# Optimization experiments

Hardware: AMD Instinct MI355X
Metric: run time of the kernel (lower is better)

The kernel has to match this reference:

```python
import jax, jax.numpy as jnp
import numpy as np

N = 50000
E = 800000
IN_C = 256
HID = 256
OUT_C = 128


def _glorot(key, fan_in, fan_out):
    lim = float(np.sqrt(6.0 / (fan_in + fan_out)))
    return jax.random.uniform(key, (fan_in, fan_out), jnp.float32, -lim, lim)


def setup_inputs() -> dict:
    key = jax.random.key(0)
    ks = jax.random.split(key, 10)
    x = jax.random.normal(ks[0], (N, IN_C), dtype=jnp.float32)
    edge_index = jax.random.randint(ks[1], (2, E), 0, N, dtype=jnp.int64)
    return {
        "x": x,
        "edge_index": edge_index,
        # layer 0 MLP: Linear(IN_C,HID)+ReLU+Linear(HID,HID)+ReLU
        "eps0": jnp.zeros((), jnp.float32),
        "W1_0": _glorot(ks[2], IN_C, HID),
        "b1_0": jnp.zeros((HID,), jnp.float32),
        "W2_0": _glorot(ks[3], HID, HID),
        "b2_0": jnp.zeros((HID,), jnp.float32),
        # layer 1 MLP: Linear(HID,HID)+ReLU+Linear(HID,OUT_C)
        "eps1": jnp.zeros((), jnp.float32),
        "W1_1": _glorot(ks[4], HID, HID),
        "b1_1": jnp.zeros((HID,), jnp.float32),
        "W2_1": _glorot(ks[5], HID, OUT_C),
        "b2_1": jnp.zeros((OUT_C,), jnp.float32),
    }


def _gin_layer(x, src, dst, eps, W1, b1, W2, b2, final_relu):
    # sum-aggregate messages x[src] into dst nodes
    agg = jax.ops.segment_sum(x[src], dst, num_segments=N)  # [N, d]
    h = (1.0 + eps) * x + agg
    h = jax.nn.relu(h @ W1 + b1)
    h = h @ W2 + b2
    return jax.nn.relu(h) if final_relu else h


def reference(x, edge_index, eps0, W1_0, b1_0, W2_0, b2_0, eps1, W1_1, b1_1, W2_1, b2_1):
    src, dst = edge_index[0], edge_index[1]
    h = _gin_layer(x, src, dst, eps0, W1_0, b1_0, W2_0, b2_0, final_relu=True)
    h = jax.nn.relu(h)  # model-level ReLU between layers
    h = _gin_layer(h, src, dst, eps1, W1_1, b1_1, W2_1, b2_1, final_relu=False)
    return jax.nn.log_softmax(h, axis=1)
```

## Files before the change

kernel.cpp:

```cpp
#include <hip/hip_runtime.h>

#define FDIM 256
#define OUTC 128
#define CAP  96
#define CURS 16
#define LDA 264
#define MROWS 128

typedef float floatx4 __attribute__((ext_vector_type(4)));
typedef __bf16 bf16x8 __attribute__((ext_vector_type(8)));

__device__ __forceinline__ unsigned short f2bf(float f) {
    union { float f; unsigned u; } v; v.f = f;
    unsigned r = v.u + 0x7FFF + ((v.u >> 16) & 1);
    return (unsigned short)(r >> 16);
}
__device__ __forceinline__ unsigned pack2(float a, float b) {
    return ((unsigned)f2bf(a)) | (((unsigned)f2bf(b)) << 16);
}
__device__ __forceinline__ unsigned q8b(float v, float rs) {
    int q = __float2int_rn(v * rs);
    q = (q < -127 ? -127 : (q > 127 ? 127 : q)) + 128;
    return (unsigned)q;
}
__device__ __forceinline__ float ub0(unsigned v) { float f; asm("v_cvt_f32_ubyte0 %0, %1" : "=v"(f) : "v"(v)); return f; }
__device__ __forceinline__ float ub1(unsigned v) { float f; asm("v_cvt_f32_ubyte1 %0, %1" : "=v"(f) : "v"(v)); return f; }
__device__ __forceinline__ float ub2(unsigned v) { float f; asm("v_cvt_f32_ubyte2 %0, %1" : "=v"(f) : "v"(v)); return f; }
__device__ __forceinline__ float ub3(unsigned v) { float f; asm("v_cvt_f32_ubyte3 %0, %1" : "=v"(f) : "v"(v)); return f; }

__global__ __launch_bounds__(256)
void prep_kernel(const int* __restrict__ src, const int* __restrict__ dst,
                 int* __restrict__ cursor, unsigned short* __restrict__ esrc2, int E,
                 const float* __restrict__ x, unsigned char* __restrict__ xq,
                 float* __restrict__ xs0, int total8,
                 const float* __restrict__ W1_0, const float* __restrict__ W2_0,
                 const float* __restrict__ W1_1, const float* __restrict__ W2_1,
                 unsigned short* __restrict__ w1f_0, unsigned short* __restrict__ w2f_0,
                 unsigned short* __restrict__ w1f_1, unsigned short* __restrict__ w2f_1) {
    int gid = blockIdx.x * 256 + threadIdx.x;
    if (gid < E) {
        int d = dst[gid];
        int pos = atomicAdd(&cursor[d * CURS], 1);
        if (pos < CAP) esrc2[d * CAP + pos] = (unsigned short)src[gid];
        return;
    }
    gid -= E;
    if (gid < total8) {
        const float4* p = (const float4*)(x + (size_t)gid * 8);
        float4 a = p[0], b = p[1];
        float m = fmaxf(fmaxf(fmaxf(fabsf(a.x), fabsf(a.y)), fmaxf(fabsf(a.z), fabsf(a.w))),
                        fmaxf(fmaxf(fabsf(b.x), fabsf(b.y)), fmaxf(fabsf(b.z), fabsf(b.w))));
        #pragma unroll
        for (int off = 1; off < 32; off <<= 1) m = fmaxf(m, __shfl_xor(m, off));
        float rs = (m > 0.f) ? 127.0f / m : 0.f;
        unsigned lo = q8b(a.x, rs) | (q8b(a.y, rs) << 8) |
                      (q8b(a.z, rs) << 16) | (q8b(a.w, rs) << 24);
        unsigned hi = q8b(b.x, rs) | (q8b(b.y, rs) << 8) |
                      (q8b(b.z, rs) << 16) | (q8b(b.w, rs) << 24);
        *(uint2*)(xq + (size_t)gid * 8) = make_uint2(lo, hi);
        if ((threadIdx.x & 31) == 0) xs0[gid >> 5] = m * (1.0f / 127.0f);
        return;
    }
    gid -= total8;
    const int S = FDIM * FDIM;
    const float* W; unsigned short* WF; int local, J, Ncols;
    if (gid < S)          { W = W1_0; WF = w1f_0; local = gid;         J = 4; Ncols = FDIM; }
    else if (gid < 2 * S) { W = W2_0; WF = w2f_0; local = gid - S;     J = 4; Ncols = FDIM; }
    else if (gid < 3 * S) { W = W1_1; WF = w1f_1; local = gid - 2 * S; J = 4; Ncols = FDIM; }
    else if (gid < 3 * S + FDIM * OUTC)
                          { W = W2_1; WF = w2f_1; local = gid - 3 * S; J = 2; Ncols = OUTC; }
    else return;
    int e    = local & 7;
    int lane = (local >> 3) & 63;
    int l15  = lane & 15;
    int quad = lane >> 4;
    int rest = local >> 9;
    int j  = rest % J;  rest /= J;
    int kc = rest & 7;
    int g  = rest >> 3;
    int n = g * (16 * J) + j * 16 + l15;
    int k = kc * 32 + quad * 8 + e;
    WF[local] = f2bf(W[(size_t)k * Ncols + n]);
}

__global__ __launch_bounds__(256)
void gather_q8_kernel(const unsigned char* __restrict__ q,
                      const float* __restrict__ qs,
                      const unsigned short* __restrict__ esrc2,
                      const int* __restrict__ cursor,
                      const float* __restrict__ epsp,
                      unsigned short* __restrict__ out, int N, float bias) {
    int node = __builtin_amdgcn_readfirstlane(
        (int)((blockIdx.x * blockDim.x + threadIdx.x) >> 6));
    int lane = threadIdx.x & 63;
    if (node >= N) return;
    int col = lane * 4;
    int beg = node * CAP;
    int cnt = cursor[node * CURS];
    if (cnt > CAP) cnt = CAP;

    float a4[4] = {0.f, 0.f, 0.f, 0.f};
    float scl_sum = 0.f;

    int e = 0;
    for (; e + 16 <= cnt; e += 16) {
        const uint4* ip = (const uint4*)(esrc2 + beg + e);
        uint4 i0 = ip[0], i1 = ip[1];
        unsigned iw[8] = {i0.x, i0.y, i0.z, i0.w, i1.x, i1.y, i1.z, i1.w};
        int s[16]; float sc[16];
        #pragma unroll
        for (int m = 0; m < 8; ++m) {
            s[2*m]   = __builtin_amdgcn_readfirstlane((int)(iw[m] & 0xffffu));
            s[2*m+1] = __builtin_amdgcn_readfirstlane((int)(iw[m] >> 16));
        }
        #pragma unroll
        for (int k = 0; k < 16; ++k) { sc[k] = qs[s[k]]; scl_sum += sc[k]; }
        unsigned v[16];
        #pragma unroll
        for (int k = 0; k < 16; ++k)
            v[k] = *(const unsigned*)(q + (size_t)s[k] * FDIM + col);
        #pragma unroll
        for (int k = 0; k < 16; ++k) {
            a4[0] = fmaf(sc[k], ub0(v[k]), a4[0]);
            a4[1] = fmaf(sc[k], ub1(v[k]), a4[1]);
            a4[2] = fmaf(sc[k], ub2(v[k]), a4[2]);
            a4[3] = fmaf(sc[k], ub3(v[k]), a4[3]);
        }
    }
    int rem = cnt - e;
    if (rem > 0) {
        const uint4* ip = (const uint4*)(esrc2 + beg + e);
        uint4 i0 = ip[0], i1 = ip[1];
        unsigned iw[8] = {i0.x, i0.y, i0.z, i0.w, i1.x, i1.y, i1.z, i1.w};
        int s[16]; float sc[16];
        #pragma unroll
        for (int m = 0; m < 8; ++m) {
            s[2*m]   = __builtin_amdgcn_readfirstlane((int)(iw[m] & 0xffffu));
            s[2*m+1] = __builtin_amdgcn_readfirstlane((int)(iw[m] >> 16));
        }
        #pragma unroll
        for (int k = 0; k < 16; ++k) if (k >= rem) s[k] = s[0];
        #pragma unroll
        for (int k = 0; k < 16; ++k) {
            sc[k] = (k < rem) ? qs[s[k]] : 0.f;
            scl_sum += sc[k];
        }
        unsigned v[16];
        #pragma unroll
        for (int k = 0; k < 16; ++k)
            v[k] = *(const unsigned*)(q + (size_t)s[k] * FDIM + col);
        #pragma unroll
        for (int k = 0; k < 16; ++k) {
            a4[0] = fmaf(sc[k], ub0(v[k]), a4[0]);
            a4[1] = fmaf(sc[k], ub1(v[k]), a4[1]);
            a4[2] = fmaf(sc[k], ub2(v[k]), a4[2]);
            a4[3] = fmaf(sc[k], ub3(v[k]), a4[3]);
        }
    }

    float ssc = qs[node] * (1.0f + *epsp);
    scl_sum += ssc;
    unsigned sv = *(const unsigned*)(q + (size_t)node * FDIM + col);
    a4[0] = fmaf(ssc, ub0(sv), a4[0]);
    a4[1] = fmaf(ssc, ub1(sv), a4[1]);
    a4[2] = fmaf(ssc, ub2(sv), a4[2]);
    a4[3] = fmaf(ssc, ub3(sv), a4[3]);

    float corr = bias * scl_sum;
    a4[0] -= corr; a4[1] -= corr; a4[2] -= corr; a4[3] -= corr;

    uint2 o;
    o.x = pack2(a4[0], a4[1]);
    o.y = pack2(a4[2], a4[3]);
    *(uint2*)(out + (size_t)node * FDIM + col) = o;
}

template<bool FINAL>
__global__ __launch_bounds__(256, 2)
void mlp_fused_kernel(const unsigned short* __restrict__ A,
                      const unsigned short* __restrict__ W1F,
                      const float* __restrict__ b1,
                      const unsigned short* __restrict__ W2F,
                      const float* __restrict__ b2,
                      void* __restrict__ Out,
                      float* __restrict__ xsp, int M) {
    extern __shared__ unsigned short As[];
    float* sred = (float*)(As + MROWS * LDA);

    int tid  = threadIdx.x;
    int wave = tid >> 6;
    int lane = tid & 63;
    int l15  = lane & 15;
    int quad = lane >> 4;
    int row0 = blockIdx.x * MROWS;

    #pragma unroll
    for (int i = 0; i < 16; ++i) {
        int idx = i * 256 + tid;
        int r = idx >> 5;
        int c = (idx & 31) * 8;
        uint4 v = make_uint4(0u, 0u, 0u, 0u);
        int gr = row0 + r;
        if (gr < M) v = *(const uint4*)(A + (size_t)gr * FDIM + c);
        *(uint4*)(As + r * LDA + c) = v;
    }
    __syncthreads();

    floatx4 zero = {0.f, 0.f, 0.f, 0.f};

    {
        floatx4 acc[8][4];
        #pragma unroll
        for (int i = 0; i < 8; ++i)
            #pragma unroll
            for (int j = 0; j < 4; ++j) acc[i][j] = zero;

        const unsigned short* Wb = W1F + (size_t)wave * 16384;
        bf16x8 bcur[4], bnxt[4];
        #pragma unroll
        for (int j = 0; j < 4; ++j)
            bcur[j] = *(const bf16x8*)(Wb + j * 512 + lane * 8);

        for (int kc = 0; kc < 8; ++kc) {
            const unsigned short* Wn = Wb + ((kc < 7) ? (kc + 1) : kc) * 2048;
            #pragma unroll
            for (int j = 0; j < 4; ++j)
                bnxt[j] = *(const bf16x8*)(Wn + j * 512 + lane * 8);
            int k = kc * 32;
            #pragma unroll
            for (int i = 0; i < 8; ++i) {
                bf16x8 af = *(const bf16x8*)(As + (i * 16 + l15) * LDA + k + quad * 8);
                #pragma unroll
                for (int j = 0; j < 4; ++j)
                    acc[i][j] = __builtin_amdgcn_mfma_f32_16x16x32_bf16(
                        af, bcur[j], acc[i][j], 0, 0, 0);
            }
            #pragma unroll
            for (int j = 0; j < 4; ++j) bcur[j] = bnxt[j];
        }

        __syncthreads();

        #pragma unroll
        for (int j = 0; j < 4; ++j) {
            int col = wave * 64 + j * 16 + l15;
            float bv = b1[col];
            #pragma unroll
            for (int i = 0; i < 8; ++i) {
                #pragma unroll
                for (int r = 0; r < 4; ++r) {
                    float v = fmaxf(acc[i][j][r] + bv, 0.f);
                    As[(i * 16 + quad * 4 + r) * LDA + col] = f2bf(v);
                }
            }
        }
    }
    __syncthreads();

    if (!FINAL) {
        floatx4 acc[8][4];
        #pragma unroll
        for (int i = 0; i < 8; ++i)
            #pragma unroll
            for (int j = 0; j < 4; ++j) acc[i][j] = zero;

        const unsigned short* Wb = W2F + (size_t)wave * 16384;
        bf16x8 bcur[4], bnxt[4];
        #pragma unroll
        for (int j = 0; j < 4; ++j)
            bcur[j] = *(const bf16x8*)(Wb + j * 512 + lane * 8);

        for (int kc = 0; kc < 8; ++kc) {
            const unsigned short* Wn = Wb + ((kc < 7) ? (kc + 1) : kc) * 2048;
            #pragma unroll
            for (int j = 0; j < 4; ++j)
                bnxt[j] = *(const bf16x8*)(Wn + j * 512 + lane * 8);
            int k = kc * 32;
            #pragma unroll
            for (int i = 0; i < 8; ++i) {
                bf16x8 af = *(const bf16x8*)(As + (i * 16 + l15) * LDA + k + quad * 8);
                #pragma unroll
                for (int j = 0; j < 4; ++j)
                    acc[i][j] = __builtin_amdgcn_mfma_f32_16x16x32_bf16(
                        af, bcur[j], acc[i][j], 0, 0, 0);
            }
            #pragma unroll
            for (int j = 0; j < 4; ++j) bcur[j] = bnxt[j];
        }

        #pragma unroll
        for (int j = 0; j < 4; ++j) {
            float bv = b2[wave * 64 + j * 16 + l15];
            #pragma unroll
            for (int i = 0; i < 8; ++i)
                #pragma unroll
                for (int r = 0; r < 4; ++r)
                    acc[i][j][r] = fmaxf(acc[i][j][r] + bv, 0.f);
        }
        #pragma unroll
        for (int i = 0; i < 8; ++i) {
            #pragma unroll
            for (int r = 0; r < 4; ++r) {
                float m = fmaxf(fmaxf(acc[i][0][r], acc[i][1][r]),
                                fmaxf(acc[i][2][r], acc[i][3][r]));
                #pragma unroll
                for (int off = 1; off < 16; off <<= 1) m = fmaxf(m, __shfl_xor(m, off));
                int row = i * 16 + quad * 4 + r;
                if (l15 == 0) sred[row * 4 + wave] = m;
            }
        }
        __syncthreads();

        unsigned char* Bq = (unsigned char*)As;
        #pragma unroll
        for (int i = 0; i < 8; ++i) {
            #pragma unroll
            for (int r = 0; r < 4; ++r) {
                int row = i * 16 + quad * 4 + r;
                float Mr = fmaxf(fmaxf(sred[row * 4 + 0], sred[row * 4 + 1]),
                                 fmaxf(sred[row * 4 + 2], sred[row * 4 + 3]));
                float rs = (Mr > 0.f) ? 255.0f / Mr : 0.f;
                if (wave == 0 && l15 == 0 && row0 + row < M)
                    xsp[row0 + row] = Mr * (1.0f / 255.0f);
                #pragma unroll
                for (int j = 0; j < 4; ++j) {
                    int col = wave * 64 + j * 16 + l15;
                    Bq[row * FDIM + col] =
                        (unsigned char)__float2int_rn(acc[i][j][r] * rs);
                }
            }
        }
        __syncthreads();

        unsigned char* Oq = (unsigned char*)Out;
        #pragma unroll
        for (int it = 0; it < 8; ++it) {
            int u4 = it * 256 + tid;
            int r = u4 >> 4;
            int gr = row0 + r;
            if (gr < M) {
                uint4 v = *(uint4*)(Bq + u4 * 16);
                *(uint4*)(Oq + (size_t)gr * FDIM + (u4 & 15) * 16) = v;
            }
        }
    } else {
        floatx4 acc[8][2];
        #pragma unroll
        for (int i = 0; i < 8; ++i)
            #pragma unroll
            for (int j = 0; j < 2; ++j) acc[i][j] = zero;

        const unsigned short* Wb = W2F + (size_t)wave * 8192;
        bf16x8 bcur[2], bnxt[2];
        #pragma unroll
        for (int j = 0; j < 2; ++j)
            bcur[j] = *(const bf16x8*)(Wb + j * 512 + lane * 8);

        for (int kc = 0; kc < 8; ++kc) {
            const unsigned short* Wn = Wb + ((kc < 7) ? (kc + 1) : kc) * 1024;
            #pragma unroll
            for (int j = 0; j < 2; ++j)
                bnxt[j] = *(const bf16x8*)(Wn + j * 512 + lane * 8);
            int k = kc * 32;
            #pragma unroll
            for (int i = 0; i < 8; ++i) {
                bf16x8 af = *(const bf16x8*)(As + (i * 16 + l15) * LDA + k + quad * 8);
                #pragma unroll
                for (int j = 0; j < 2; ++j)
                    acc[i][j] = __builtin_amdgcn_mfma_f32_16x16x32_bf16(
                        af, bcur[j], acc[i][j], 0, 0, 0);
            }
            #pragma unroll
            for (int j = 0; j < 2; ++j) bcur[j] = bnxt[j];
        }

        #pragma unroll
        for (int j = 0; j < 2; ++j) {
            float bv = b2[wave * 32 + j * 16 + l15];
            #pragma unroll
            for (int i = 0; i < 8; ++i)
                #pragma unroll
                for (int r = 0; r < 4; ++r) acc[i][j][r] += bv;
        }

        float* smax = sred;
        float* ssum = sred + MROWS * 4;

        #pragma unroll
        for (int i = 0; i < 8; ++i) {
            #pragma unroll
            for (int r = 0; r < 4; ++r) {
                float m = fmaxf(acc[i][0][r], acc[i][1][r]);
                #pragma unroll
                for (int off = 1; off < 16; off <<= 1) m = fmaxf(m, __shfl_xor(m, off));
                int row = i * 16 + quad * 4 + r;
                if (l15 == 0) smax[row * 4 + wave] = m;
            }
        }
        __syncthreads();

        float Mloc[8][4];
        #pragma unroll
        for (int i = 0; i < 8; ++i) {
            #pragma unroll
            for (int r = 0; r < 4; ++r) {
                int row = i * 16 + quad * 4 + r;
                float Mr = fmaxf(fmaxf(smax[row * 4 + 0], smax[row * 4 + 1]),
                                 fmaxf(smax[row * 4 + 2], smax[row * 4 + 3]));
                Mloc[i][r] = Mr;
                float s = __expf(acc[i][0][r] - Mr) + __expf(acc[i][1][r] - Mr);
                #pragma unroll
                for (int off = 1; off < 16; off <<= 1) s += __shfl_xor(s, off);
                if (l15 == 0) ssum[row * 4 + wave] = s;
            }
        }
        __syncthreads();

        float* O = (float*)Out;
        #pragma unroll
        for (int i = 0; i < 8; ++i) {
            #pragma unroll
            for (int r = 0; r < 4; ++r) {
                int row = i * 16 + quad * 4 + r;
                int grow = row0 + row;
                if (grow < M) {
                    float lse = Mloc[i][r] +
                        __logf(ssum[row * 4 + 0] + ssum[row * 4 + 1] +
                               ssum[row * 4 + 2] + ssum[row * 4 + 3]);
                    #pragma unroll
                    for (int j = 0; j < 2; ++j) {
                        int col = wave * 32 + j * 16 + l15;
                        O[(size_t)grow * OUTC + col] = acc[i][j][r] - lse;
                    }
                }
            }
        }
    }
}

extern "C" void kernel_launch(void* const* d_in, const int* in_sizes, int n_in,
                              void* d_out, int out_size, void* d_ws, size_t ws_size,
                              hipStream_t stream) {
    const float* x    = (const float*)d_in[0];
    const int*   ei   = (const int*)d_in[1];
    const float* eps0 = (const float*)d_in[2];
    const float* W1_0 = (const float*)d_in[3];
    const float* b1_0 = (const float*)d_in[4];
    const float* W2_0 = (const float*)d_in[5];
    const float* b2_0 = (const float*)d_in[6];
    const float* eps1 = (const float*)d_in[7];
    const float* W1_1 = (const float*)d_in[8];
    const float* b1_1 = (const float*)d_in[9];
    const float* W2_1 = (const float*)d_in[10];
    const float* b2_1 = (const float*)d_in[11];
    float* out = (float*)d_out;

    const int N = in_sizes[0] / FDIM;
    const int E = in_sizes[1] / 2;
    const int* src = ei;
    const int* dst = ei + E;

    size_t buf_elems = (size_t)N * FDIM;
    unsigned short* agg   = (unsigned short*)d_ws;
    float*          xs0   = (float*)(agg + buf_elems);
    float*          xs1   = xs0 + N;
    int*            cursor= (int*)(xs1 + N);
    unsigned short* esrc2 = (unsigned short*)(cursor + (size_t)N * CURS);
    unsigned short* w1f_0 = esrc2 + (size_t)N * CAP;
    unsigned short* w2f_0 = w1f_0 + FDIM * FDIM;
    unsigned short* w1f_1 = w2f_0 + FDIM * FDIM;
    unsigned short* w2f_1 = w1f_1 + FDIM * FDIM;
    unsigned char*  xq    = (unsigned char*)(w2f_1 + FDIM * OUTC);
    unsigned char*  h2q   = xq + buf_elems;

    int gather_blocks = (N + 3) / 4;
    int mlp_blocks = (N + MROWS - 1) / MROWS;
    int total8 = (int)(buf_elems / 8);
    int wtot = 3 * FDIM * FDIM + FDIM * OUTC;
    int prep_threads = E + total8 + wtot;
    size_t mlp_lds = (size_t)MROWS * LDA * 2 + (size_t)MROWS * 4 * 2 * 4;

    hipMemsetAsync(cursor, 0, (size_t)N * CURS * sizeof(int), stream);
    prep_kernel<<<(prep_threads + 255) / 256, 256, 0, stream>>>(
        src, dst, cursor, esrc2, E, x, xq, xs0, total8,
        W1_0, W2_0, W1_1, W2_1, w1f_0, w2f_0, w1f_1, w2f_1);

    gather_q8_kernel<<<gather_blocks, 256, 0, stream>>>(
        xq, xs0, esrc2, cursor, eps0, agg, N, 128.0f);
    mlp_fused_kernel<false><<<mlp_blocks, 256, mlp_lds, stream>>>(
        agg, w1f_0, b1_0, w2f_0, b2_0, h2q, xs1, N);

    gather_q8_kernel<<<gather_blocks, 256, 0, stream>>>(
        h2q, xs1, esrc2, cursor, eps1, agg, N, 0.0f);
    mlp_fused_kernel<true><<<mlp_blocks, 256, mlp_lds, stream>>>(
        agg, w1f_1, b1_1, w2f_1, b2_1, out, nullptr, N);
}
```

Before: 287.4 us.

## Stage MLP weight slices into LDS with double-buffered direct loads and halve row tile

The fused MLP kernel now copies each k-slice of the bf16 weights into a double-buffered LDS region using global_load_lds, prefetching the next slice while MFMAs run on the current one. Before, each wave loaded its weights straight from global memory into registers. The row tile shrinks from 128 to 64 rows, which halves accumulator registers and roughly doubles the block count for better occupancy. The weight pre-swizzle in the prep kernel is reordered to k-major so that each staged slice is contiguous. In exchange, every k step now has a full vmcnt wait and a block barrier, and weights are re-read from global memory by twice as many blocks.

Measured after the change: 292.9 us. Within noise of the previous version (+1.9%).

```diff
diff --git a/kernel.cpp b/kernel.cpp
--- a/kernel.cpp
+++ b/kernel.cpp
@@ -5,7 +5,7 @@
 #define CAP  96
 #define CURS 16
 #define LDA 264
-#define MROWS 128
+#define MROWS 64
 
 typedef float floatx4 __attribute__((ext_vector_type(4)));
 typedef __bf16 bf16x8 __attribute__((ext_vector_type(8)));
@@ -27,6 +27,12 @@
 __device__ __forceinline__ float ub1(unsigned v) { float f; asm("v_cvt_f32_ubyte1 %0, %1" : "=v"(f) : "v"(v)); return f; }
 __device__ __forceinline__ float ub2(unsigned v) { float f; asm("v_cvt_f32_ubyte2 %0, %1" : "=v"(f) : "v"(v)); return f; }
 __device__ __forceinline__ float ub3(unsigned v) { float f; asm("v_cvt_f32_ubyte3 %0, %1" : "=v"(f) : "v"(v)); return f; }
+
+__device__ __forceinline__ void gl2lds16(const void* g, void* l) {
+    __builtin_amdgcn_global_load_lds(
+        (const __attribute__((address_space(1))) unsigned int*)g,
+        (__attribute__((address_space(3))) unsigned int*)l, 16, 0, 0);
+}
 
 __global__ __launch_bounds__(256)
 void prep_kernel(const int* __restrict__ src, const int* __restrict__ dst,
@@ -74,10 +80,10 @@
     int lane = (local >> 3) & 63;
     int l15  = lane & 15;
     int quad = lane >> 4;
-    int rest = local >> 9;
-    int j  = rest % J;  rest /= J;
-    int kc = rest & 7;
-    int g  = rest >> 3;
+    int t  = local >> 9;
+    int j  = t % J;  t /= J;
+    int g  = t & 3;
+    int kc = t >> 2;
     int n = g * (16 * J) + j * 16 + l15;
     int k = kc * 32 + quad * 8 + e;
     WF[local] = f2bf(W[(size_t)k * Ncols + n]);
@@ -184,8 +190,9 @@
                       const float* __restrict__ b2,
                       void* __restrict__ Out,
                       float* __restrict__ xsp, int M) {
-    extern __shared__ unsigned short As[];
-    float* sred = (float*)(As + MROWS * LDA);
+    __shared__ unsigned short As[MROWS * LDA];
+    __shared__ unsigned short Bs[2][8192];
+    __shared__ float sred[MROWS * 4 * 2];
 
     int tid  = threadIdx.x;
     int wave = tid >> 6;
@@ -194,8 +201,17 @@
     int quad = lane >> 4;
     int row0 = blockIdx.x * MROWS;
 
+    auto stageB = [&](const unsigned short* WF, int kcs, int buf, int sliceB) {
+        const char* gs = (const char*)WF + (size_t)kcs * sliceB;
+        char* ls = (char*)Bs[buf];
+        int myg = wave * 1024 + lane * 16;
+        int myl = wave * 1024;
+        for (int r = 0; r < (sliceB >> 12); ++r)
+            gl2lds16(gs + r * 4096 + myg, ls + r * 4096 + myl);
+    };
+
     #pragma unroll
-    for (int i = 0; i < 16; ++i) {
+    for (int i = 0; i < 8; ++i) {
         int idx = i * 256 + tid;
         int r = idx >> 5;
         int c = (idx & 31) * 8;
@@ -204,49 +220,50 @@
         if (gr < M) v = *(const uint4*)(A + (size_t)gr * FDIM + c);
         *(uint4*)(As + r * LDA + c) = v;
     }
+    int cur = 0;
+    stageB(W1F, 0, 0, 16384);
+    asm volatile("s_waitcnt vmcnt(0)" ::: "memory");
     __syncthreads();
 
     floatx4 zero = {0.f, 0.f, 0.f, 0.f};
 
     {
-        floatx4 acc[8][4];
-        #pragma unroll
-        for (int i = 0; i < 8; ++i)
+        floatx4 acc[4][4];
+        #pragma unroll
+        for (int i = 0; i < 4; ++i)
             #pragma unroll
             for (int j = 0; j < 4; ++j) acc[i][j] = zero;
 
-        const unsigned short* Wb = W1F + (size_t)wave * 16384;
-        bf16x8 bcur[4], bnxt[4];
-        #pragma unroll
-        for (int j = 0; j < 4; ++j)
-            bcur[j] = *(const bf16x8*)(Wb + j * 512 + lane * 8);
-
         for (int kc = 0; kc < 8; ++kc) {
-            const unsigned short* Wn = Wb + ((kc < 7) ? (kc + 1) : kc) * 2048;
+            if (kc < 7) stageB(W1F, kc + 1, cur ^ 1, 16384);
+            const unsigned short* Bc = Bs[cur] + wave * 2048;
+            bf16x8 bf[4], af[4];
             #pragma unroll
             for (int j = 0; j < 4; ++j)
-                bnxt[j] = *(const bf16x8*)(Wn + j * 512 + lane * 8);
+                bf[j] = *(const bf16x8*)(Bc + j * 512 + lane * 8);
             int k = kc * 32;
             #pragma unroll
-            for (int i = 0; i < 8; ++i) {
-                bf16x8 af = *(const bf16x8*)(As + (i * 16 + l15) * LDA + k + quad * 8);
+            for (int i = 0; i < 4; ++i)
+                af[i] = *(const bf16x8*)(As + (i * 16 + l15) * LDA + k + quad * 8);
+            #pragma unroll
+            for (int i = 0; i < 4; ++i)
                 #pragma unroll
                 for (int j = 0; j < 4; ++j)
                     acc[i][j] = __builtin_amdgcn_mfma_f32_16x16x32_bf16(
-                        af, bcur[j], acc[i][j], 0, 0, 0);
-            }
-            #pragma unroll
-            for (int j = 0; j < 4; ++j) bcur[j] = bnxt[j];
-        }
-
-        __syncthreads();
+                        af[i], bf[j], acc[i][j], 0, 0, 0);
+            asm volatile("s_waitcnt vmcnt(0)" ::: "memory");
+            __syncthreads();
+            cur ^= 1;
+        }
+
+        stageB(W2F, 0, cur, FINAL ? 8192 : 16384);
 
         #pragma unroll
         for (int j = 0; j < 4; ++j) {
             int col = wave * 64 + j * 16 + l15;
             float bv = b1[col];
             #pragma unroll
-            for (int i = 0; i < 8; ++i) {
+            for (int i = 0; i < 4; ++i) {
                 #pragma unroll
                 for (int r = 0; r < 4; ++r) {
                     float v = fmaxf(acc[i][j][r] + bv, 0.f);
@@ -255,50 +272,49 @@
             }
         }
     }
+    asm volatile("s_waitcnt vmcnt(0)" ::: "memory");
     __syncthreads();
 
     if (!FINAL) {
-        floatx4 acc[8][4];
-        #pragma unroll
-        for (int i = 0; i < 8; ++i)
+        floatx4 acc[4][4];
+        #pragma unroll
+        for (int i = 0; i < 4; ++i)
             #pragma unroll
             for (int j = 0; j < 4; ++j) acc[i][j] = zero;
 
-        const unsigned short* Wb = W2F + (size_t)wave * 16384;
-        bf16x8 bcur[4], bnxt[4];
-        #pragma unroll
-        for (int j = 0; j < 4; ++j)
-            bcur[j] = *(const bf16x8*)(Wb + j * 512 + lane * 8);
-
         for (int kc = 0; kc < 8; ++kc) {
-            const unsigned short* Wn = Wb + ((kc < 7) ? (kc + 1) : kc) * 2048;
+            if (kc < 7) stageB(W2F, kc + 1, cur ^ 1, 16384);
+            const unsigned short* Bc = Bs[cur] + wave * 2048;
+            bf16x8 bf[4], af[4];
             #pragma unroll
             for (int j = 0; j < 4; ++j)
-                bnxt[j] = *(const bf16x8*)(Wn + j * 512 + lane * 8);
+                bf[j] = *(const bf16x8*)(Bc + j * 512 + lane * 8);
             int k = kc * 32;
             #pragma unroll
-            for (int i = 0; i < 8; ++i) {
-                bf16x8 af = *(const bf16x8*)(As + (i * 16 + l15) * LDA + k + quad * 8);
+            for (int i = 0; i < 4; ++i)
+                af[i] = *(const bf16x8*)(As + (i * 16 + l15) * LDA + k + quad * 8);
+            #pragma unroll
+            for (int i = 0; i < 4; ++i)
                 #pragma unroll
                 for (int j = 0; j < 4; ++j)
                     acc[i][j] = __builtin_amdgcn_mfma_f32_16x16x32_bf16(
-                        af, bcur[j], acc[i][j], 0, 0, 0);
-            }
-            #pragma unroll
-            for (int j = 0; j < 4; ++j) bcur[j] = bnxt[j];
+                        af[i], bf[j], acc[i][j], 0, 0, 0);
+            asm volatile("s_waitcnt vmcnt(0)" ::: "memory");
+            __syncthreads();
+            cur ^= 1;
         }
 
         #pragma unroll
         for (int j = 0; j < 4; ++j) {
             float bv = b2[wave * 64 + j * 16 + l15];
             #pragma unroll
-            for (int i = 0; i < 8; ++i)
+            for (int i = 0; i < 4; ++i)
                 #pragma unroll
                 for (int r = 0; r < 4; ++r)
                     acc[i][j][r] = fmaxf(acc[i][j][r] + bv, 0.f);
         }
         #pragma unroll
-        for (int i = 0; i < 8; ++i) {
+        for (int i = 0; i < 4; ++i) {
             #pragma unroll
             for (int r = 0; r < 4; ++r) {
                 float m = fmaxf(fmaxf(acc[i][0][r], acc[i][1][r]),
@@ -313,7 +329,7 @@
 
         unsigned char* Bq = (unsigned char*)As;
         #pragma unroll
-        for (int i = 0; i < 8; ++i) {
+        for (int i = 0; i < 4; ++i) {
             #pragma unroll
             for (int r = 0; r < 4; ++r) {
                 int row = i * 16 + quad * 4 + r;
@@ -334,7 +350,7 @@
 
         unsigned char* Oq = (unsigned char*)Out;
         #pragma unroll
-        for (int it = 0; it < 8; ++it) {
+        for (int it = 0; it < 4; ++it) {
             int u4 = it * 256 + tid;
             int r = u4 >> 4;
             int gr = row0 + r;
@@ -344,41 +360,39 @@
             }
         }
     } else {
-        floatx4 acc[8][2];
-        #pragma unroll
-        for (int i = 0; i < 8; ++i)
+        floatx4 acc[4][2];
+        #pragma unroll
+        for (int i = 0; i < 4; ++i)
             #pragma unroll
             for (int j = 0; j < 2; ++j) acc[i][j] = zero;
 
-        const unsigned short* Wb = W2F + (size_t)wave * 8192;
-        bf16x8 bcur[2], bnxt[2];
-        #pragma unroll
-        for (int j = 0; j < 2; ++j)
-            bcur[j] = *(const bf16x8*)(Wb + j * 512 + lane * 8);
-
         for (int kc = 0; kc < 8; ++kc) {
-            const unsigned short* Wn = Wb + ((kc < 7) ? (kc + 1) : kc) * 1024;
+            if (kc < 7) stageB(W2F, kc + 1, cur ^ 1, 8192);
+            const unsigned short* Bc = Bs[cur] + wave * 1024;
+            bf16x8 bf[2], af[4];
             #pragma unroll
             for (int j = 0; j < 2; ++j)
-                bnxt[j] = *(const bf16x8*)(Wn + j * 512 + lane * 8);
+                bf[j] = *(const bf16x8*)(Bc + j * 512 + lane * 8);
             int k = kc * 32;
             #pragma unroll
-            for (int i = 0; i < 8; ++i) {
-                bf16x8 af = *(const bf16x8*)(As + (i * 16 + l15) * LDA + k + quad * 8);
+            for (int i = 0; i < 4; ++i)
+                af[i] = *(const bf16x8*)(As + (i * 16 + l15) * LDA + k + quad * 8);
+            #pragma unroll
+            for (int i = 0; i < 4; ++i)
                 #pragma unroll
                 for (int j = 0; j < 2; ++j)
                     acc[i][j] = __builtin_amdgcn_mfma_f32_16x16x32_bf16(
-                        af, bcur[j], acc[i][j], 0, 0, 0);
-            }
-            #pragma unroll
-            for (int j = 0; j < 2; ++j) bcur[j] = bnxt[j];
+                        af[i], bf[j], acc[i][j], 0, 0, 0);
+            asm volatile("s_waitcnt vmcnt(0)" ::: "memory");
+            __syncthreads();
+            cur ^= 1;
         }
 
         #pragma unroll
         for (int j = 0; j < 2; ++j) {
             float bv = b2[wave * 32 + j * 16 + l15];
             #pragma unroll
-            for (int i = 0; i < 8; ++i)
+            for (int i = 0; i < 4; ++i)
                 #pragma unroll
                 for (int r = 0; r < 4; ++r) acc[i][j][r] += bv;
         }
@@ -387,7 +401,7 @@
         float* ssum = sred + MROWS * 4;
 
         #pragma unroll
-        for (int i = 0; i < 8; ++i) {
+        for (int i = 0; i < 4; ++i) {
             #pragma unroll
             for (int r = 0; r < 4; ++r) {
                 float m = fmaxf(acc[i][0][r], acc[i][1][r]);
@@ -399,9 +413,9 @@
         }
         __syncthreads();
 
-        float Mloc[8][4];
-        #pragma unroll
-        for (int i = 0; i < 8; ++i) {
+        float Mloc[4][4];
+        #pragma unroll
+        for (int i = 0; i < 4; ++i) {
             #pragma unroll
             for (int r = 0; r < 4; ++r) {
                 int row = i * 16 + quad * 4 + r;
@@ -418,7 +432,7 @@
 
         float* O = (float*)Out;
         #pragma unroll
-        for (int i = 0; i < 8; ++i) {
+        for (int i = 0; i < 4; ++i) {
             #pragma unroll
             for (int r = 0; r < 4; ++r) {
                 int row = i * 16 + quad * 4 + r;
@@ -478,7 +492,6 @@
     int total8 = (int)(buf_elems / 8);
     int wtot = 3 * FDIM * FDIM + FDIM * OUTC;
     int prep_threads = E + total8 + wtot;
-    size_t mlp_lds = (size_t)MROWS * LDA * 2 + (size_t)MROWS * 4 * 2 * 4;
 
     hipMemsetAsync(cursor, 0, (size_t)N * CURS * sizeof(int), stream);
     prep_kernel<<<(prep_threads + 255) / 256, 256, 0, stream>>>(
@@ -487,11 +500,11 @@
 
     gather_q8_kernel<<<gather_blocks, 256, 0, stream>>>(
         xq, xs0, esrc2, cursor, eps0, agg, N, 128.0f);
-    mlp_fused_kernel<false><<<mlp_blocks, 256, mlp_lds, stream>>>(
+    mlp_fused_kernel<false><<<mlp_blocks, 256, 0, stream>>>(
         agg, w1f_0, b1_0, w2f_0, b2_0, h2q, xs1, N);
 
     gather_q8_kernel<<<gather_blocks, 256, 0, stream>>>(
         h2q, xs1, esrc2, cursor, eps1, agg, N, 0.0f);
-    mlp_fused_kernel<true><<<mlp_blocks, 256, mlp_lds, stream>>>(
+    mlp_fused_kernel<true><<<mlp_blocks, 256, 0, stream>>>(
         agg, w1f_1, b1_1, w2f_1, b2_1, out, nullptr, N);
 }
```
